# Optimization experiments

Hardware: AMD Instinct MI355X
Metric: run time of the kernel (lower is better)

The kernel has to match this reference:

```python
import jax, jax.numpy as jnp
import numpy as np

B, D, C, S = 65536, 128, 10, 2
LAMBDA_E, LAMBDA_OD = 0.1, 0.036
GAMMA_E, GAMMA_OD = 2.0, 2.0
STEP_SIZE = 1000.0


def setup_inputs() -> dict:
    key = jax.random.key(0)
    ks = jax.random.split(key, 12)
    inp = {
        "mean_t": jax.random.normal(ks[0], (B, D), jnp.float32),
        "mean_s": jax.random.normal(ks[1], (B, D), jnp.float32),
        "log_std_t": jax.random.normal(ks[2], (B, D), jnp.float32),
        "log_std_s": jax.random.normal(ks[3], (B, D), jnp.float32),
        "y_zt": jax.random.normal(ks[4], (B, C), jnp.float32),
        "s_zt": jax.random.normal(ks[5], (B, S), jnp.float32),
        "eps_prior_t": jax.random.normal(ks[6], (B, D), jnp.float32),
        "eps_prior_s": jax.random.normal(ks[7], (B, D), jnp.float32),
        "eps_t": jax.random.normal(ks[8], (B, D), jnp.float32),
        "eps_s": jax.random.normal(ks[9], (B, D), jnp.float32),
        "target": jax.random.randint(ks[10], (B,), 0, C, jnp.int64),
        "current_step": 500,
    }
    return inp


def _kld_batchmean(log_p, t):
    # torch KLDivLoss(reduction='batchmean'): sum(t * (log t - log_p)) / batch
    return jnp.sum(t * (jnp.log(t) - log_p)) / t.shape[0]


def reference(mean_t, mean_s, log_std_t, log_std_s, y_zt, s_zt,
              eps_prior_t, eps_prior_s, eps_t, eps_s, target, current_step):
    # CIFAR10 branch: cross entropy on task logits
    logp_y = jax.nn.log_softmax(y_zt, axis=1)
    L_t = -jnp.mean(jnp.take_along_axis(logp_y, target[:, None], axis=1))

    # entropy loss on sensitive discriminator output
    sm = jax.nn.softmax(s_zt, axis=1)
    lsm = jax.nn.log_softmax(s_zt, axis=1)
    Loss_e = -jnp.sum(sm * lsm) / s_zt.shape[0]

    # prior samples: N(0, I) and N(1, I)  (mean_tensors(zeros, ones))
    prior_t = eps_prior_t            # mean 0
    prior_s = 1.0 + eps_prior_s      # mean 1

    # encoder samples: MVN(mean, diag(exp(log_std))) -> std = exp(0.5*log_std)
    # torch .sample() is non-differentiable -> stop_gradient
    enc_t = jax.lax.stop_gradient(mean_t + jnp.exp(0.5 * log_std_t) * eps_t)
    enc_s = jax.lax.stop_gradient(mean_s + jnp.exp(0.5 * log_std_s) * eps_s)

    L_zt = _kld_batchmean(jax.nn.log_softmax(prior_t, axis=1), jax.nn.softmax(enc_t, axis=1))
    L_zs = _kld_batchmean(jax.nn.log_softmax(prior_s, axis=1), jax.nn.softmax(enc_s, axis=1))

    frac = current_step / STEP_SIZE
    lam_e = LAMBDA_E * GAMMA_E ** frac
    lam_od = LAMBDA_OD * GAMMA_OD ** frac
    return L_t + lam_e * Loss_e + lam_od * (L_zt + L_zs)
```

## Files before the change

kernel.cpp:

```cpp
#include <hip/hip_runtime.h>
#include <hip/hip_bf16.h>
#include <math.h>

#define BATCH 65536
#define NCLS  10
#define NKL   2048
#define NCE   64
#define NBTOT (NKL + NCE)

typedef float vf4 __attribute__((ext_vector_type(4)));


__global__ __launch_bounds__(256, 2) void crit_main(
    const float* __restrict__ mean_t,      const float* __restrict__ mean_s,
    const float* __restrict__ log_std_t,   const float* __restrict__ log_std_s,
    const float* __restrict__ y_zt,        const float* __restrict__ s_zt,
    const float* __restrict__ eps_prior_t, const float* __restrict__ eps_prior_s,
    const float* __restrict__ eps_t,       const float* __restrict__ eps_s,
    const int*   __restrict__ target,
    double*      __restrict__ ws_partial)
{
    const int tid = threadIdx.x;
    double ce_d = 0.0, H_d = 0.0, kl_d = 0.0;

    if (blockIdx.x < NKL) {
        const int lane = tid & 63;
        const int sub  = lane & 15;
        const int grp  = (lane >> 4) & 3;
        const int gwave = blockIdx.x * 4 + (tid >> 6);
        const int rowbase = gwave * 8;

        const vf4* MT = (const vf4*)mean_t;
        const vf4* LT = (const vf4*)log_std_t;
        const vf4* ET = (const vf4*)eps_t;
        const vf4* PT = (const vf4*)eps_prior_t;
        const vf4* MS = (const vf4*)mean_s;
        const vf4* LS = (const vf4*)log_std_s;
        const vf4* ES = (const vf4*)eps_s;
        const vf4* PS = (const vf4*)eps_prior_s;

        int i0[2], i1[2];
        #pragma unroll
        for (int k = 0; k < 2; ++k) {
            const int row = rowbase + k * 4 + grp;
            i0[k] = row * 32 + sub;
            i1[k] = i0[k] + 16;
        }

        vf4 mt[2][2], lt[2][2], et[2][2], pt[2][2];
        vf4 ms[2][2], ls[2][2], es[2][2], ps[2][2];
        #pragma unroll
        for (int k = 0; k < 2; ++k) {
            mt[k][0] = __builtin_nontemporal_load(&MT[i0[k]]);
            mt[k][1] = __builtin_nontemporal_load(&MT[i1[k]]);
            lt[k][0] = __builtin_nontemporal_load(&LT[i0[k]]);
            lt[k][1] = __builtin_nontemporal_load(&LT[i1[k]]);
            et[k][0] = __builtin_nontemporal_load(&ET[i0[k]]);
            et[k][1] = __builtin_nontemporal_load(&ET[i1[k]]);
            pt[k][0] = __builtin_nontemporal_load(&PT[i0[k]]);
            pt[k][1] = __builtin_nontemporal_load(&PT[i1[k]]);
            ms[k][0] = __builtin_nontemporal_load(&MS[i0[k]]);
            ms[k][1] = __builtin_nontemporal_load(&MS[i1[k]]);
            ls[k][0] = __builtin_nontemporal_load(&LS[i0[k]]);
            ls[k][1] = __builtin_nontemporal_load(&LS[i1[k]]);
            es[k][0] = __builtin_nontemporal_load(&ES[i0[k]]);
            es[k][1] = __builtin_nontemporal_load(&ES[i1[k]]);
            ps[k][0] = __builtin_nontemporal_load(&PS[i0[k]]);
            ps[k][1] = __builtin_nontemporal_load(&PS[i1[k]]);
        }
        __builtin_amdgcn_sched_barrier(0);

        float red[2][6];
        #pragma unroll
        for (int k = 0; k < 2; ++k) {
            #pragma unroll
            for (int j = 0; j < 6; ++j) red[k][j] = 0.0f;
            #pragma unroll
            for (int h = 0; h < 2; ++h) {
                #pragma unroll
                for (int c = 0; c < 4; ++c) {
                    const float enc_t = fmaf(__expf(0.5f * lt[k][h][c]), et[k][h][c], mt[k][h][c]);
                    const float enc_s = fmaf(__expf(0.5f * ls[k][h][c]), es[k][h][c], ms[k][h][c]);
                    const float xt = __expf(enc_t);
                    const float xs = __expf(enc_s);
                    red[k][0] += xt;
                    red[k][1] += __expf(pt[k][h][c]);
                    red[k][2] += xt * (enc_t - pt[k][h][c]);
                    red[k][3] += xs;
                    red[k][4] += __expf(ps[k][h][c]);
                    red[k][5] += xs * (enc_s - ps[k][h][c]);
                }
            }
        }

        #pragma unroll
        for (int m = 8; m >= 1; m >>= 1) {
            #pragma unroll
            for (int k = 0; k < 2; ++k) {
                #pragma unroll
                for (int j = 0; j < 6; ++j) red[k][j] += __shfl_xor(red[k][j], m, 64);
            }
        }

        float kl = 0.0f;
        #pragma unroll
        for (int k = 0; k < 2; ++k) {
            const float rt = 1.0f / red[k][0];
            const float rs = 1.0f / red[k][3];
            kl += red[k][2] * rt + __logf(red[k][1] * rt)
                + red[k][5] * rs + __logf(red[k][4] * rs);
        }
        kl_d = (sub == 0) ? (double)kl : 0.0;
    } else {
        const int gtid = (blockIdx.x - NKL) * 256 + tid;
        #pragma unroll
        for (int k = 0; k < 4; ++k) {
            const int r = gtid + k * 16384;
            const float* yr = y_zt + (size_t)r * NCLS;
            const float2 y0 = *(const float2*)(yr + 0);
            const float2 y1 = *(const float2*)(yr + 2);
            const float2 y2 = *(const float2*)(yr + 4);
            const float2 y3 = *(const float2*)(yr + 6);
            const float2 y4 = *(const float2*)(yr + 8);
            const float2 s2 = *(const float2*)(s_zt + (size_t)r * 2);
            const int    t  = target[r];

            float yt = y0.x;
            yt = (t == 1) ? y0.y : yt;
            yt = (t == 2) ? y1.x : yt;
            yt = (t == 3) ? y1.y : yt;
            yt = (t == 4) ? y2.x : yt;
            yt = (t == 5) ? y2.y : yt;
            yt = (t == 6) ? y3.x : yt;
            yt = (t == 7) ? y3.y : yt;
            yt = (t == 8) ? y4.x : yt;
            yt = (t == 9) ? y4.y : yt;

            const float Z = (__expf(y0.x) + __expf(y0.y))
                          + (__expf(y1.x) + __expf(y1.y))
                          + (__expf(y2.x) + __expf(y2.y))
                          + (__expf(y3.x) + __expf(y3.y))
                          + (__expf(y4.x) + __expf(y4.y));
            ce_d += (double)(__logf(Z) - yt);

            const float za = __expf(s2.x), zb = __expf(s2.y);
            const float Zs = za + zb;
            const float lses = __logf(Zs);
            H_d += (double)(-((za / Zs) * (s2.x - lses) + (zb / Zs) * (s2.y - lses)));
        }
    }

    __shared__ double sred[256][3];
    sred[tid][0] = ce_d; sred[tid][1] = H_d; sred[tid][2] = kl_d;
    __syncthreads();
    #pragma unroll
    for (int s = 128; s > 0; s >>= 1) {
        if (tid < s) {
            sred[tid][0] += sred[tid + s][0];
            sred[tid][1] += sred[tid + s][1];
            sred[tid][2] += sred[tid + s][2];
        }
        __syncthreads();
    }
    if (tid == 0) {
        ws_partial[blockIdx.x * 3 + 0] = sred[0][0];
        ws_partial[blockIdx.x * 3 + 1] = sred[0][1];
        ws_partial[blockIdx.x * 3 + 2] = sred[0][2];
    }
}

__global__ __launch_bounds__(256) void crit_reduce(
    const double* __restrict__ ws_partial,
    const int*    __restrict__ step_ptr,
    float*        __restrict__ out,
    int nblocks)
{
    const int tid = threadIdx.x;
    double c = 0.0, h = 0.0, k = 0.0;
    for (int i = tid; i < nblocks; i += 256) {
        c += ws_partial[3 * i + 0];
        h += ws_partial[3 * i + 1];
        k += ws_partial[3 * i + 2];
    }
    __shared__ double sc[256], sh_[256], sk[256];
    sc[tid] = c; sh_[tid] = h; sk[tid] = k;
    __syncthreads();
    for (int s = 128; s > 0; s >>= 1) {
        if (tid < s) { sc[tid] += sc[tid + s]; sh_[tid] += sh_[tid + s]; sk[tid] += sk[tid + s]; }
        __syncthreads();
    }
    if (tid == 0) {
        double frac  = (double)step_ptr[0] / 1000.0;
        double lam_e  = 0.1   * exp2(frac);
        double lam_od = 0.036 * exp2(frac);
        out[0] = (float)((sc[0] + lam_e * sh_[0] + lam_od * sk[0]) / (double)BATCH);
    }
}

extern "C" void kernel_launch(void* const* d_in, const int* in_sizes, int n_in,
                              void* d_out, int out_size, void* d_ws, size_t ws_size,
                              hipStream_t stream) {
    const float* mean_t      = (const float*)d_in[0];
    const float* mean_s      = (const float*)d_in[1];
    const float* log_std_t   = (const float*)d_in[2];
    const float* log_std_s   = (const float*)d_in[3];
    const float* y_zt        = (const float*)d_in[4];
    const float* s_zt        = (const float*)d_in[5];
    const float* eps_prior_t = (const float*)d_in[6];
    const float* eps_prior_s = (const float*)d_in[7];
    const float* eps_t       = (const float*)d_in[8];
    const float* eps_s       = (const float*)d_in[9];
    const int*   target      = (const int*)d_in[10];
    const int*   step_ptr    = (const int*)d_in[11];

    double* ws_partial = (double*)d_ws;
    float*  out        = (float*)d_out;

    crit_main<<<NBTOT, 256, 0, stream>>>(
        mean_t, mean_s, log_std_t, log_std_s, y_zt, s_zt,
        eps_prior_t, eps_prior_s, eps_t, eps_s, target, ws_partial);
    crit_reduce<<<1, 256, 0, stream>>>(ws_partial, step_ptr, out, NBTOT);
}
```

Baseline: 239.4 us.

## Replace block shared-memory reduction with per-wave shuffle partials and reorder blocks

```diff
diff --git a/kernel.cpp b/kernel.cpp
--- a/kernel.cpp
+++ b/kernel.cpp
@@ -1,12 +1,14 @@
 #include <hip/hip_runtime.h>
-#include <hip/hip_bf16.h>
 #include <math.h>
 
 #define BATCH 65536
 #define NCLS  10
+#define NCE   64
 #define NKL   2048
-#define NCE   64
 #define NBTOT (NKL + NCE)
+#define KL_WAVES (NKL * 4)
+#define CE_WAVES (NCE * 4)
+
 
 typedef float vf4 __attribute__((ext_vector_type(4)));
 
@@ -21,13 +23,13 @@
     double*      __restrict__ ws_partial)
 {
     const int tid = threadIdx.x;
-    double ce_d = 0.0, H_d = 0.0, kl_d = 0.0;
-
-    if (blockIdx.x < NKL) {
-        const int lane = tid & 63;
+    const int wid = tid >> 6;
+    const int lane = tid & 63;
+
+    if (blockIdx.x >= NCE) {
         const int sub  = lane & 15;
         const int grp  = (lane >> 4) & 3;
-        const int gwave = blockIdx.x * 4 + (tid >> 6);
+        const int gwave = (blockIdx.x - NCE) * 4 + wid;
         const int rowbase = gwave * 8;
 
         const vf4* MT = (const vf4*)mean_t;
@@ -69,6 +71,15 @@
             ps[k][1] = __builtin_nontemporal_load(&PS[i1[k]]);
         }
         __builtin_amdgcn_sched_barrier(0);
+        asm volatile("" ::
+            "v"(mt[0][0]), "v"(mt[0][1]), "v"(mt[1][0]), "v"(mt[1][1]),
+            "v"(lt[0][0]), "v"(lt[0][1]), "v"(lt[1][0]), "v"(lt[1][1]),
+            "v"(et[0][0]), "v"(et[0][1]), "v"(et[1][0]), "v"(et[1][1]),
+            "v"(pt[0][0]), "v"(pt[0][1]), "v"(pt[1][0]), "v"(pt[1][1]),
+            "v"(ms[0][0]), "v"(ms[0][1]), "v"(ms[1][0]), "v"(ms[1][1]),
+            "v"(ls[0][0]), "v"(ls[0][1]), "v"(ls[1][0]), "v"(ls[1][1]),
+            "v"(es[0][0]), "v"(es[0][1]), "v"(es[1][0]), "v"(es[1][1]),
+            "v"(ps[0][0]), "v"(ps[0][1]), "v"(ps[1][0]), "v"(ps[1][1]));
 
         float red[2][6];
         #pragma unroll
@@ -110,9 +121,12 @@
             kl += red[k][2] * rt + __logf(red[k][1] * rt)
                 + red[k][5] * rs + __logf(red[k][4] * rs);
         }
-        kl_d = (sub == 0) ? (double)kl : 0.0;
+        kl += __shfl_xor(kl, 16, 64);
+        kl += __shfl_xor(kl, 32, 64);
+        if (lane == 0) ws_partial[gwave] = (double)kl;
     } else {
-        const int gtid = (blockIdx.x - NKL) * 256 + tid;
+        double ce_d = 0.0, H_d = 0.0;
+        const int gtid = blockIdx.x * 256 + tid;
         #pragma unroll
         for (int k = 0; k < 4; ++k) {
             const int r = gtid + k * 16384;
@@ -148,40 +162,31 @@
             const float lses = __logf(Zs);
             H_d += (double)(-((za / Zs) * (s2.x - lses) + (zb / Zs) * (s2.y - lses)));
         }
-    }
-
-    __shared__ double sred[256][3];
-    sred[tid][0] = ce_d; sred[tid][1] = H_d; sred[tid][2] = kl_d;
-    __syncthreads();
-    #pragma unroll
-    for (int s = 128; s > 0; s >>= 1) {
-        if (tid < s) {
-            sred[tid][0] += sred[tid + s][0];
-            sred[tid][1] += sred[tid + s][1];
-            sred[tid][2] += sred[tid + s][2];
-        }
-        __syncthreads();
-    }
-    if (tid == 0) {
-        ws_partial[blockIdx.x * 3 + 0] = sred[0][0];
-        ws_partial[blockIdx.x * 3 + 1] = sred[0][1];
-        ws_partial[blockIdx.x * 3 + 2] = sred[0][2];
+
+        #pragma unroll
+        for (int m = 32; m >= 1; m >>= 1) {
+            ce_d += __shfl_xor(ce_d, m, 64);
+            H_d  += __shfl_xor(H_d,  m, 64);
+        }
+        if (lane == 0) {
+            const int cw = blockIdx.x * 4 + wid;
+            ws_partial[KL_WAVES + cw]            = ce_d;
+            ws_partial[KL_WAVES + CE_WAVES + cw] = H_d;
+        }
     }
 }
 
 __global__ __launch_bounds__(256) void crit_reduce(
     const double* __restrict__ ws_partial,
     const int*    __restrict__ step_ptr,
-    float*        __restrict__ out,
-    int nblocks)
+    float*        __restrict__ out)
 {
     const int tid = threadIdx.x;
-    double c = 0.0, h = 0.0, k = 0.0;
-    for (int i = tid; i < nblocks; i += 256) {
-        c += ws_partial[3 * i + 0];
-        h += ws_partial[3 * i + 1];
-        k += ws_partial[3 * i + 2];
-    }
+    double k = 0.0;
+    for (int i = tid; i < KL_WAVES; i += 256) k += ws_partial[i];
+    double c = ws_partial[KL_WAVES + tid];
+    double h = ws_partial[KL_WAVES + CE_WAVES + tid];
+
     __shared__ double sc[256], sh_[256], sk[256];
     sc[tid] = c; sh_[tid] = h; sk[tid] = k;
     __syncthreads();
@@ -219,5 +224,5 @@
     crit_main<<<NBTOT, 256, 0, stream>>>(
         mean_t, mean_s, log_std_t, log_std_s, y_zt, s_zt,
         eps_prior_t, eps_prior_s, eps_t, eps_s, target, ws_partial);
-    crit_reduce<<<1, 256, 0, stream>>>(ws_partial, step_ptr, out, NBTOT);
+    crit_reduce<<<1, 256, 0, stream>>>(ws_partial, step_ptr, out);
 }
```

After: 244.7 us. 1.02x slower.
